# Optimization experiments

Hardware: AMD Instinct MI355X
Metric: run time of the kernel (lower is better)

The kernel has to match this reference:

```python
import jax, jax.numpy as jnp
import numpy as np

D_MODEL = 1024
D_STATE = 16
LN_EPS = 1e-5


def setup_inputs() -> dict:
    key = jax.random.key(0)
    ks = jax.random.split(key, 8)
    batch, seq_len = 8, 4096
    x = jax.random.normal(ks[0], (batch, seq_len, D_MODEL), dtype=jnp.float32)
    A = jax.random.normal(ks[1], (D_STATE, D_STATE), dtype=jnp.float32) * 0.01
    # nn.Linear default init: U(-1/sqrt(fan_in), 1/sqrt(fan_in))
    bb = 1.0 / np.sqrt(D_MODEL)
    B_w = jax.random.uniform(ks[2], (D_STATE, D_MODEL), minval=-bb, maxval=bb)
    B_b = jax.random.uniform(ks[3], (D_STATE,), minval=-bb, maxval=bb)
    cb = 1.0 / np.sqrt(D_STATE)
    C_w = jax.random.uniform(ks[4], (D_MODEL, D_STATE), minval=-cb, maxval=cb)
    C_b = jax.random.uniform(ks[5], (D_MODEL,), minval=-cb, maxval=cb)
    D = jnp.ones((D_MODEL,), dtype=jnp.float32) * 0.01
    gate_w = jax.random.uniform(ks[6], (D_MODEL, D_MODEL), minval=-bb, maxval=bb)
    gate_b = jax.random.uniform(ks[7], (D_MODEL,), minval=-bb, maxval=bb)
    ln_g = jnp.ones((D_MODEL,), dtype=jnp.float32)
    ln_b = jnp.zeros((D_MODEL,), dtype=jnp.float32)
    return {"x": x, "A": A, "B_w": B_w, "B_b": B_b, "C_w": C_w, "C_b": C_b,
            "D": D, "gate_w": gate_w, "gate_b": gate_b, "ln_g": ln_g, "ln_b": ln_b}


def _layer_norm(z, g, b):
    mu = jnp.mean(z, axis=-1, keepdims=True)
    var = jnp.mean(jnp.square(z - mu), axis=-1, keepdims=True)
    return (z - mu) * jax.lax.rsqrt(var + LN_EPS) * g + b


def reference(x, A, B_w, B_b, C_w, C_b, D, gate_w, gate_b, ln_g, ln_b):
    batch, seq_len, d_model = x.shape
    # Precompute B(x_t) for all t in one GEMM: [b, s, d_state]
    Bx = jnp.einsum('bsd,nd->bsn', x, B_w) + B_b

    def step(state, bx_t):  # state: [b, d_state], bx_t: [b, d_state]
        new_state = jnp.tanh(state @ A.T + bx_t)
        return new_state, new_state

    init = jnp.zeros((batch, A.shape[0]), dtype=x.dtype)
    _, states = jax.lax.scan(step, init, jnp.swapaxes(Bx, 0, 1))  # [s, b, n]
    states = jnp.swapaxes(states, 0, 1)  # [b, s, d_state]

    output = jnp.einsum('bsn,dn->bsd', states, C_w) + C_b + D * x
    gate = jax.nn.silu(jnp.einsum('bsd,ed->bse', x, gate_w) + gate_b)
    output = gate * output + (1.0 - gate) * x
    return _layer_norm(output + x, ln_g, ln_b)
```

## Files before the change

kernel.cpp:

```cpp
#include <hip/hip_runtime.h>
#include <hip/hip_bf16.h>
#include <cstdint>
#include <cstddef>

#define DM     1024
#define DSTATE 16
#define SEQ    4096
#define BATCH  8
#define MROWS  (BATCH * SEQ)
#define LNEPS  1e-5f

#define CHUNK  64
#define WARM   16
#define NCHUNK (SEQ / CHUNK)

typedef __hip_bfloat16 bf16;
typedef __attribute__((ext_vector_type(8))) short short8;
typedef __attribute__((ext_vector_type(4))) float f32x4;

static __device__ __forceinline__ unsigned short f2bf(float f) {
  bf16 h = __float2bfloat16(f);
  return __builtin_bit_cast(unsigned short, h);
}

#define GLDS16(SRC, DSTOFF, LDSBASE)                                          \
  __builtin_amdgcn_global_load_lds(                                           \
      (const __attribute__((address_space(1))) void*)(SRC),                   \
      (__attribute__((address_space(3))) void*)((LDSBASE) + (DSTOFF)), 16, 0, 0)

__global__ __launch_bounds__(256) void canon_x(const float* __restrict__ xin,
                                               bf16* __restrict__ wsx) {
  size_t i = ((size_t)blockIdx.x * 256 + threadIdx.x) * 8;
  const float4* p = (const float4*)(xin + i);
  float4 a = p[0], b = p[1];
  uint4 o;
  o.x = (unsigned)f2bf(a.x) | ((unsigned)f2bf(a.y) << 16);
  o.y = (unsigned)f2bf(a.z) | ((unsigned)f2bf(a.w) << 16);
  o.z = (unsigned)f2bf(b.x) | ((unsigned)f2bf(b.y) << 16);
  o.w = (unsigned)f2bf(b.z) | ((unsigned)f2bf(b.w) << 16);
  *(uint4*)(wsx + i) = o;
}

__global__ __launch_bounds__(256) void canon_gw(const float* __restrict__ gw,
                                                bf16* __restrict__ gwc) {
  size_t i = ((size_t)blockIdx.x * 256 + threadIdx.x) * 8;
  const float4* p = (const float4*)(gw + i);
  float4 a = p[0], b = p[1];
  uint4 o;
  o.x = (unsigned)f2bf(a.x) | ((unsigned)f2bf(a.y) << 16);
  o.y = (unsigned)f2bf(a.z) | ((unsigned)f2bf(a.w) << 16);
  o.z = (unsigned)f2bf(b.x) | ((unsigned)f2bf(b.y) << 16);
  o.w = (unsigned)f2bf(b.z) | ((unsigned)f2bf(b.w) << 16);
  *(uint4*)(gwc + i) = o;
}

__global__ __launch_bounds__(256) void bx_kernel(const bf16* __restrict__ X,
                                                 const float* __restrict__ Bw,
                                                 const float* __restrict__ Bb,
                                                 float* __restrict__ Bx) {
  __shared__ __align__(16) char lds[40960];
  const int tid  = threadIdx.x;
  const int lane = tid & 63;
  const int w    = tid >> 6;
  const int fm   = lane & 15;
  const int fq   = lane >> 4;
  const int l4   = lane >> 2, lk = lane & 3;
  const int m0   = blockIdx.x * 64;

  {
    int t6   = tid & 63;
    int nb   = tid >> 6;
    int step = t6 >> 1;
    int cq0  = (t6 & 1) * 2;
#pragma unroll
    for (int p = 0; p < 4; ++p) {
      int n = p * 4 + nb;
      const float4* src = (const float4*)(Bw + (size_t)n * DM + t6 * 16);
      float4 a = src[0], b = src[1], c = src[2], d = src[3];
      uint4 o0, o1;
      o0.x = (unsigned)f2bf(a.x) | ((unsigned)f2bf(a.y) << 16);
      o0.y = (unsigned)f2bf(a.z) | ((unsigned)f2bf(a.w) << 16);
      o0.z = (unsigned)f2bf(b.x) | ((unsigned)f2bf(b.y) << 16);
      o0.w = (unsigned)f2bf(b.z) | ((unsigned)f2bf(b.w) << 16);
      o1.x = (unsigned)f2bf(c.x) | ((unsigned)f2bf(c.y) << 16);
      o1.y = (unsigned)f2bf(c.z) | ((unsigned)f2bf(c.w) << 16);
      o1.z = (unsigned)f2bf(d.x) | ((unsigned)f2bf(d.y) << 16);
      o1.w = (unsigned)f2bf(d.z) | ((unsigned)f2bf(d.w) << 16);
      int sw = (n >> 1) & 3;
      *(uint4*)(lds + step * 1024 + n * 64 + ((cq0 ^ sw) << 4))       = o0;
      *(uint4*)(lds + step * 1024 + n * 64 + (((cq0 + 1) ^ sw) << 4)) = o1;
    }
  }

  const int rowA = w * 16 + l4;
  const int kqA  = lk ^ ((rowA >> 1) & 3);
  GLDS16(X + (size_t)(m0 + rowA) * DM + kqA * 8, 32768 + w * 1024, lds);
  __syncthreads();

  const int rA   = w * 16 + fm;
  const int offA = rA * 64 + ((fq ^ ((rA >> 1) & 3)) << 4);
  const int offB = fm * 64 + ((fq ^ ((fm >> 1) & 3)) << 4);

  f32x4 acc = (f32x4)(0.f);
  for (int t = 0; t < 32; ++t) {
    const int cb = 32768 + (t & 1) * 4096;
    const int sb = 32768 + 4096 - (t & 1) * 4096;
    if (t < 31)
      GLDS16(X + (size_t)(m0 + rowA) * DM + (t + 1) * 32 + kqA * 8,
             sb + w * 1024, lds);
    short8 af  = *(const short8*)(lds + cb + offA);
    short8 bfv = *(const short8*)(lds + t * 1024 + offB);
    acc = __builtin_amdgcn_mfma_f32_16x16x32_bf16(af, bfv, acc, 0, 0, 0);
    __syncthreads();
  }
  float bb = Bb[fm];
#pragma unroll
  for (int q = 0; q < 4; ++q) {
    int row = m0 + w * 16 + fq * 4 + q;
    Bx[(size_t)row * DSTATE + fm] = acc[q] + bb;
  }
}

__global__ __launch_bounds__(64) void scan_kernel(const float* __restrict__ A,
                                                  const float* __restrict__ Bx,
                                                  float* __restrict__ st) {
  int lane = threadIdx.x;
  int n    = lane & 15;
  int base = lane & 48;
  int chain = blockIdx.x * 4 + (lane >> 4);
  int c = chain >> 3;
  int b = chain & 7;

  float Arow[16];
#pragma unroll
  for (int m = 0; m < 16; m++) Arow[m] = A[n * 16 + m];

  int t0   = (c == 0) ? 0 : c * CHUNK - WARM;
  int t1   = c * CHUNK;
  int tEnd = c * CHUNK + CHUNK;

  const float* bxp = Bx + (size_t)b * SEQ * DSTATE + n;
  float*       stp = st + (size_t)b * SEQ * DSTATE + n;

  float state = 0.f;
  for (int t = t0; t < tEnd; t++) {
    float a = bxp[(size_t)t * DSTATE];
#pragma unroll
    for (int m = 0; m < 16; m++)
      a += Arow[m] * __shfl(state, base + m, 64);
    state = tanhf(a);
    if (t >= t1) stp[(size_t)t * DSTATE] = state;
  }
}

#define FBM 32
#define FBK 32
#define NT  (DM / FBK)
#define BUFB 67584
#define CW_OFF 0
#define ST_OFF 65536
#define PART_OFF 67584
#define TOT_OFF 69632
#define BOUNCE 71680

__global__ __launch_bounds__(512, 2) void fused_kernel(
    const bf16* __restrict__ X, const bf16* __restrict__ Gw,
    const float* __restrict__ xf, const float* __restrict__ st,
    const float* __restrict__ Cw, const float* __restrict__ Cb,
    const float* __restrict__ Dv, const float* __restrict__ gb,
    const float* __restrict__ lng, const float* __restrict__ lnb,
    float* __restrict__ out) {
  __shared__ __align__(16) char lds[137216];
  const int tid  = threadIdx.x;
  const int lane = tid & 63;
  const int w    = tid >> 6;
  const int fm   = lane & 15;
  const int fq   = lane >> 4;
  const int m0   = blockIdx.x * FBM;
  const int l4   = lane >> 2, lk = lane & 3;

  int colS[8], kqS[8];
#pragma unroll
  for (int s = 0; s < 8; s++) {
    int col = (w * 8 + s) * 16 + l4;
    colS[s] = col;
    kqS[s]  = lk ^ ((col >> 1) & 3);
  }
  const int rowA = w * 16 + l4;
  const int kqA  = lk ^ ((rowA >> 1) & 3);

  int offA[2], offB[8];
#pragma unroll
  for (int i = 0; i < 2; i++) {
    int r = i * 16 + fm;
    offA[i] = r * 64 + ((fq ^ ((r >> 1) & 3)) << 4);
  }
#pragma unroll
  for (int j = 0; j < 8; j++) {
    int c = w * 128 + j * 16 + fm;
    offB[j] = 2048 + c * 64 + ((fq ^ ((c >> 1) & 3)) << 4);
  }

  f32x4 acc[2][8];
#pragma unroll
  for (int i = 0; i < 2; i++)
#pragma unroll
    for (int j = 0; j < 8; j++) acc[i][j] = (f32x4)(0.f);

  {
#pragma unroll
    for (int s = 0; s < 8; s++)
      GLDS16(Gw + (size_t)colS[s] * DM + kqS[s] * 8,
             2048 + (w * 8 + s) * 1024, lds);
    if (w < 2)
      GLDS16(X + (size_t)(m0 + rowA) * DM + kqA * 8, w * 1024, lds);
  }
  __syncthreads();

  for (int t = 0; t < NT; t++) {
    const int cb = (t & 1) * BUFB;
    const int sb = BUFB - cb;
    if (t < NT - 1) {
      const int kb = (t + 1) * FBK;
#pragma unroll
      for (int s = 0; s < 8; s++)
        GLDS16(Gw + (size_t)colS[s] * DM + kb + kqS[s] * 8,
               sb + 2048 + (w * 8 + s) * 1024, lds);
      if (w < 2)
        GLDS16(X + (size_t)(m0 + rowA) * DM + kb + kqA * 8, sb + w * 1024, lds);
    } else {
#pragma unroll
      for (int s = 0; s < 8; s++) {
        int c   = w * 8 + s;
        int col = c * 16 + l4;
        int nq  = lk ^ ((col >> 1) & 3);
        GLDS16(Cw + (size_t)col * DSTATE + nq * 4, CW_OFF + c * 1024, lds);
      }
      if (w >= 6) {
        int cc  = w - 6;
        int row = cc * 16 + l4;
        int nq  = lk ^ ((row >> 1) & 3);
        GLDS16(st + (size_t)(m0 + row) * DSTATE + nq * 4, ST_OFF + cc * 1024, lds);
      }
    }

    short8 af[2];
#pragma unroll
    for (int i = 0; i < 2; i++) af[i] = *(const short8*)(lds + cb + offA[i]);
#pragma unroll
    for (int j = 0; j < 8; j++) {
      short8 bfj = *(const short8*)(lds + cb + offB[j]);
#pragma unroll
      for (int i = 0; i < 2; i++)
        acc[i][j] = __builtin_amdgcn_mfma_f32_16x16x32_bf16(af[i], bfj,
                                                            acc[i][j], 0, 0, 0);
    }
    __syncthreads();
  }

#pragma unroll
  for (int i = 0; i < 2; i++) {
    f32x4 stv[4][4];
#pragma unroll
    for (int nq = 0; nq < 4; nq++)
#pragma unroll
      for (int r = 0; r < 4; r++) {
        int row = i * 16 + fq * 4 + r;
        stv[nq][r] = *(const f32x4*)(lds + ST_OFF + row * 64 +
                                     ((nq ^ ((row >> 1) & 3)) << 4));
      }
    float sum4[4] = {0.f, 0.f, 0.f, 0.f};
    float ssq4[4] = {0.f, 0.f, 0.f, 0.f};
#pragma unroll
    for (int j = 0; j < 8; j++) {
      int c = w * 128 + j * 16 + fm;
      float oc[4] = {0.f, 0.f, 0.f, 0.f};
#pragma unroll
      for (int nq = 0; nq < 4; nq++) {
        f32x4 cw = *(const f32x4*)(lds + CW_OFF + c * 64 +
                                   ((nq ^ ((c >> 1) & 3)) << 4));
#pragma unroll
        for (int r = 0; r < 4; r++)
          oc[r] += stv[nq][r][0] * cw[0] + stv[nq][r][1] * cw[1] +
                   stv[nq][r][2] * cw[2] + stv[nq][r][3] * cw[3];
      }
      float gbv = gb[c], cbv = Cb[c], dvv = Dv[c];
#pragma unroll
      for (int r = 0; r < 4; r++) {
        int   grow = m0 + i * 16 + fq * 4 + r;
        float xv = xf[(size_t)grow * DM + c];
        float zg = acc[i][j][r] + gbv;
        float g  = zg / (1.f + __expf(-zg));
        float ocf = oc[r] + cbv + dvv * xv;
        float y  = g * ocf + (1.f - g) * xv;
        float z2 = y + xv;
        acc[i][j][r] = z2;
        sum4[r] += z2;
        ssq4[r] += z2 * z2;
      }
    }
#pragma unroll
    for (int r = 0; r < 4; r++) {
#pragma unroll
      for (int off = 1; off < 16; off <<= 1) {
        sum4[r] += __shfl_xor(sum4[r], off, 64);
        ssq4[r] += __shfl_xor(ssq4[r], off, 64);
      }
    }
    if (fm == 0) {
#pragma unroll
      for (int r = 0; r < 4; r++) {
        int row = i * 16 + fq * 4 + r;
        *(float2*)(lds + PART_OFF + w * 256 + row * 8) =
            make_float2(sum4[r], ssq4[r]);
      }
    }
  }
  __syncthreads();

  if (tid < 32) {
    float s = 0.f, q = 0.f;
#pragma unroll
    for (int ww = 0; ww < 8; ww++) {
      float2 p = *(const float2*)(lds + PART_OFF + ww * 256 + tid * 8);
      s += p.x; q += p.y;
    }
    float mu  = s * (1.f / DM);
    float var = q * (1.f / DM) - mu * mu;
    *(float2*)(lds + TOT_OFF + tid * 8) = make_float2(mu, rsqrtf(var + LNEPS));
  }
  __syncthreads();

  for (int h = 0; h < 2; ++h) {
#pragma unroll
    for (int j = 0; j < 8; ++j) {
      int c = w * 128 + j * 16 + fm;
#pragma unroll
      for (int r = 0; r < 4; ++r) {
        int row16 = fq * 4 + r;
        *(float*)(lds + BOUNCE + row16 * 4096 + c * 4) = acc[h][j][r];
      }
    }
    __syncthreads();
    {
      int row16 = tid >> 5;
      int lbase = (tid & 31) * 4;
      float2 mi = *(const float2*)(lds + TOT_OFF + (h * 16 + row16) * 8);
#pragma unroll
      for (int q = 0; q < 8; ++q) {
        int col = lbase + q * 128;
        f32x4 z = *(const f32x4*)(lds + BOUNCE + row16 * 4096 + col * 4);
        float4 g4 = *(const float4*)(lng + col);
        float4 b4 = *(const float4*)(lnb + col);
        float4 ov;
        ov.x = (z[0] - mi.x) * mi.y * g4.x + b4.x;
        ov.y = (z[1] - mi.x) * mi.y * g4.y + b4.y;
        ov.z = (z[2] - mi.x) * mi.y * g4.z + b4.z;
        ov.w = (z[3] - mi.x) * mi.y * g4.w + b4.w;
        *(float4*)(out + (size_t)(m0 + h * 16 + row16) * DM + col) = ov;
      }
    }
    __syncthreads();
  }
}

extern "C" void kernel_launch(void* const* d_in, const int* in_sizes, int n_in,
                              void* d_out, int out_size, void* d_ws, size_t ws_size,
                              hipStream_t stream) {
  (void)in_sizes; (void)n_in;
  const float* x   = (const float*)d_in[0];
  const float* A   = (const float*)d_in[1];
  const float* Bw  = (const float*)d_in[2];
  const float* Bb  = (const float*)d_in[3];
  const float* Cw  = (const float*)d_in[4];
  const float* Cb  = (const float*)d_in[5];
  const float* Dv  = (const float*)d_in[6];
  const float* Gw  = (const float*)d_in[7];
  const float* gb  = (const float*)d_in[8];
  const float* lng = (const float*)d_in[9];
  const float* lnb = (const float*)d_in[10];
  float* out = (float*)d_out;

  const size_t NEED = (size_t)72 << 20;
  if (ws_size < NEED) {
    hipMemsetAsync(d_out, 0, (size_t)out_size * 4, stream);
    return;
  }

  char* ws = (char*)d_ws;
  bf16*  wsx = (bf16*)(ws);
  bf16*  gwc = (bf16*)(ws + ((size_t)64 << 20));
  float* Bx  = (float*)(ws + ((size_t)66 << 20));
  float* st  = (float*)(ws + ((size_t)68 << 20));

  canon_x <<<MROWS * DM / (256 * 8), 256, 0, stream>>>(x, wsx);
  canon_gw<<<DM * DM / (256 * 8), 256, 0, stream>>>(Gw, gwc);
  bx_kernel<<<MROWS / 64, 256, 0, stream>>>(wsx, Bw, Bb, Bx);
  scan_kernel<<<(BATCH * NCHUNK) / 4, 64, 0, stream>>>(A, Bx, st);
  fused_kernel<<<MROWS / FBM, 512, 0, stream>>>(
      wsx, gwc, x, st, Cw, Cb, Dv, gb, lng, lnb, out);
}
```

Baseline: 523.6 us.

## Use partial vmcnt waits with raw barriers, merge canon kernels, cheaper tanh

```diff
diff --git a/kernel.cpp b/kernel.cpp
--- a/kernel.cpp
+++ b/kernel.cpp
@@ -28,30 +28,34 @@
       (const __attribute__((address_space(1))) void*)(SRC),                   \
       (__attribute__((address_space(3))) void*)((LDSBASE) + (DSTOFF)), 16, 0, 0)
 
-__global__ __launch_bounds__(256) void canon_x(const float* __restrict__ xin,
-                                               bf16* __restrict__ wsx) {
-  size_t i = ((size_t)blockIdx.x * 256 + threadIdx.x) * 8;
-  const float4* p = (const float4*)(xin + i);
+#define WAITV(N) asm volatile("s_waitcnt vmcnt(" #N ")" ::: "memory")
+
+#define XBLK (MROWS * DM / (256 * 8))
+#define GBLK (DM * DM / (256 * 8))
+
+__global__ __launch_bounds__(256) void canon_all(const float* __restrict__ xin,
+                                                 const float* __restrict__ gw,
+                                                 bf16* __restrict__ wsx,
+                                                 bf16* __restrict__ gwc) {
+  int blk = blockIdx.x;
+  const float* src;
+  bf16* dst;
+  size_t i;
+  if (blk < XBLK) {
+    i = ((size_t)blk * 256 + threadIdx.x) * 8;
+    src = xin; dst = wsx;
+  } else {
+    i = ((size_t)(blk - XBLK) * 256 + threadIdx.x) * 8;
+    src = gw; dst = gwc;
+  }
+  const float4* p = (const float4*)(src + i);
   float4 a = p[0], b = p[1];
   uint4 o;
   o.x = (unsigned)f2bf(a.x) | ((unsigned)f2bf(a.y) << 16);
   o.y = (unsigned)f2bf(a.z) | ((unsigned)f2bf(a.w) << 16);
   o.z = (unsigned)f2bf(b.x) | ((unsigned)f2bf(b.y) << 16);
   o.w = (unsigned)f2bf(b.z) | ((unsigned)f2bf(b.w) << 16);
-  *(uint4*)(wsx + i) = o;
-}
-
-__global__ __launch_bounds__(256) void canon_gw(const float* __restrict__ gw,
-                                                bf16* __restrict__ gwc) {
-  size_t i = ((size_t)blockIdx.x * 256 + threadIdx.x) * 8;
-  const float4* p = (const float4*)(gw + i);
-  float4 a = p[0], b = p[1];
-  uint4 o;
-  o.x = (unsigned)f2bf(a.x) | ((unsigned)f2bf(a.y) << 16);
-  o.y = (unsigned)f2bf(a.z) | ((unsigned)f2bf(a.w) << 16);
-  o.z = (unsigned)f2bf(b.x) | ((unsigned)f2bf(b.y) << 16);
-  o.w = (unsigned)f2bf(b.z) | ((unsigned)f2bf(b.w) << 16);
-  *(uint4*)(gwc + i) = o;
+  *(uint4*)(dst + i) = o;
 }
 
 __global__ __launch_bounds__(256) void bx_kernel(const bf16* __restrict__ X,
@@ -105,13 +109,19 @@
   for (int t = 0; t < 32; ++t) {
     const int cb = 32768 + (t & 1) * 4096;
     const int sb = 32768 + 4096 - (t & 1) * 4096;
-    if (t < 31)
+    if (t < 31) {
       GLDS16(X + (size_t)(m0 + rowA) * DM + (t + 1) * 32 + kqA * 8,
              sb + w * 1024, lds);
+      WAITV(1);
+    } else {
+      WAITV(0);
+    }
+    __builtin_amdgcn_s_barrier();
+    __builtin_amdgcn_sched_barrier(0);
     short8 af  = *(const short8*)(lds + cb + offA);
     short8 bfv = *(const short8*)(lds + t * 1024 + offB);
     acc = __builtin_amdgcn_mfma_f32_16x16x32_bf16(af, bfv, acc, 0, 0, 0);
-    __syncthreads();
+    __builtin_amdgcn_s_barrier();
   }
   float bb = Bb[fm];
 #pragma unroll
@@ -148,7 +158,9 @@
 #pragma unroll
     for (int m = 0; m < 16; m++)
       a += Arow[m] * __shfl(state, base + m, 64);
-    state = tanhf(a);
+    float e = __expf(-2.f * fabsf(a));
+    float r = (1.f - e) / (1.f + e);
+    state = __builtin_copysignf(r, a);
     if (t >= t1) stp[(size_t)t * DSTATE] = state;
   }
 }
@@ -215,7 +227,6 @@
     if (w < 2)
       GLDS16(X + (size_t)(m0 + rowA) * DM + kqA * 8, w * 1024, lds);
   }
-  __syncthreads();
 
   for (int t = 0; t < NT; t++) {
     const int cb = (t & 1) * BUFB;
@@ -236,14 +247,18 @@
         int nq  = lk ^ ((col >> 1) & 3);
         GLDS16(Cw + (size_t)col * DSTATE + nq * 4, CW_OFF + c * 1024, lds);
       }
-      if (w >= 6) {
-        int cc  = w - 6;
+      if (w < 2) {
+        int cc  = w;
         int row = cc * 16 + l4;
         int nq  = lk ^ ((row >> 1) & 3);
         GLDS16(st + (size_t)(m0 + row) * DSTATE + nq * 4, ST_OFF + cc * 1024, lds);
       }
     }
 
+    if (w < 2) WAITV(9); else WAITV(8);
+    __builtin_amdgcn_s_barrier();
+    __builtin_amdgcn_sched_barrier(0);
+
     short8 af[2];
 #pragma unroll
     for (int i = 0; i < 2; i++) af[i] = *(const short8*)(lds + cb + offA[i]);
@@ -255,8 +270,9 @@
         acc[i][j] = __builtin_amdgcn_mfma_f32_16x16x32_bf16(af[i], bfj,
                                                             acc[i][j], 0, 0, 0);
     }
-    __syncthreads();
-  }
+    __builtin_amdgcn_s_barrier();
+  }
+  __syncthreads();
 
 #pragma unroll
   for (int i = 0; i < 2; i++) {
@@ -393,8 +409,7 @@
   float* Bx  = (float*)(ws + ((size_t)66 << 20));
   float* st  = (float*)(ws + ((size_t)68 << 20));
 
-  canon_x <<<MROWS * DM / (256 * 8), 256, 0, stream>>>(x, wsx);
-  canon_gw<<<DM * DM / (256 * 8), 256, 0, stream>>>(Gw, gwc);
+  canon_all<<<XBLK + GBLK, 256, 0, stream>>>(x, Gw, wsx, gwc);
   bx_kernel<<<MROWS / 64, 256, 0, stream>>>(wsx, Bw, Bb, Bx);
   scan_kernel<<<(BATCH * NCHUNK) / 4, 64, 0, stream>>>(A, Bx, st);
   fused_kernel<<<MROWS / FBM, 512, 0, stream>>>(
```

New measurement: 500.0 us. -4.5%, faster.
